# Performance work log

Hardware: AMD Instinct MI355X
Metric: run time of the kernel (lower is better)

Reference implementation:

```python
import jax, jax.numpy as jnp
import numpy as np

N_WIRES = 4
DIM = 2 ** N_WIRES          # 16-dim state vector
N_OPS = 30                  # RandomLayer(n_ops=30)
GAMMA = 1.0
ALPHA = 0.5
C64 = jnp.complex64


def _rx_mat(t):
    h = t / 2
    c = jnp.cos(h).astype(C64)
    s = (-1j * jnp.sin(h)).astype(C64)
    return jnp.stack([jnp.stack([c, s]), jnp.stack([s, c])])


def _ry_mat(t):
    h = t / 2
    c = jnp.cos(h).astype(C64)
    s = jnp.sin(h).astype(C64)
    return jnp.stack([jnp.stack([c, -s]), jnp.stack([s, c])])


def _rz_mat(t):
    h = (t / 2).astype(C64)
    z = jnp.zeros((), C64)
    return jnp.stack([jnp.stack([jnp.exp(-1j * h), z]), jnp.stack([z, jnp.exp(1j * h)])])


def _embed(g, w):
    # kron(I_{2^w}, g, I_{2^{n-1-w}}); wire 0 = most significant qubit
    return jnp.kron(jnp.kron(jnp.eye(2 ** w, dtype=C64), g),
                    jnp.eye(2 ** (N_WIRES - 1 - w), dtype=C64))


def _cnot_full(c, t):
    m = np.zeros((DIM, DIM), np.complex64)
    for i in range(DIM):
        j = i ^ (1 << (N_WIRES - 1 - t)) if (i >> (N_WIRES - 1 - c)) & 1 else i
        m[j, i] = 1.0
    return jnp.asarray(m)


def fixed_unitary(rand_angles, rx_param, ry_param):
    """Compose the whole batch-independent gate sequence (random layer +
    per-wire trainable RX/RY) into one 16x16 unitary — the 'fused kernel'."""
    U = jnp.eye(DIM, dtype=C64)
    for i in range(N_OPS):
        t, w = i % 4, i % N_WIRES
        if t == 0:
            g = _embed(_rx_mat(rand_angles[i]), w)
        elif t == 1:
            g = _embed(_ry_mat(rand_angles[i]), w)
        elif t == 2:
            g = _embed(_rz_mat(rand_angles[i]), w)
        else:
            g = _cnot_full(w, (w + 1) % N_WIRES)
        U = g @ U
    for w in range(N_WIRES):
        U = _embed(_rx_mat(rx_param[0]), w) @ U
        U = _embed(_ry_mat(ry_param[0]), w) @ U
    return U


def encode_ry(state, angles):
    """GeneralEncoder '4xRy': apply RY(angles[:, w]) on wire w, batched."""
    B = state.shape[0]
    for w in range(N_WIRES):
        h = angles[:, w] / 2
        c = jnp.cos(h).astype(C64)[:, None, None]
        s = jnp.sin(h).astype(C64)[:, None, None]
        st = state.reshape(B, 2 ** w, 2, 2 ** (N_WIRES - 1 - w))
        s0, s1 = st[:, :, 0, :], st[:, :, 1, :]
        state = jnp.stack([c * s0 - s * s1, s * s0 + c * s1], axis=2).reshape(B, DIM)
    return state


def setup_inputs() -> dict:
    key = jax.random.key(0)
    k1, k2, k3, k4, k5 = jax.random.split(key, 5)
    B = 1048576
    return {
        "x": jax.random.normal(k1, (B, 4), dtype=jnp.float32),
        "y": jax.random.normal(k2, (B, 4), dtype=jnp.float32),
        "rand_angles": jax.random.uniform(k3, (30,), dtype=jnp.float32),
        "rx_param": jax.random.normal(k4, (1,), dtype=jnp.float32),
        "ry_param": jax.random.normal(k5, (1,), dtype=jnp.float32),
    }


def reference(x, y, rand_angles, rx_param, ry_param):
    B = x.shape[0]
    # classical RBF kernel, [B, 1]
    diff = x - y
    rbf = jnp.exp(-GAMMA * jnp.sum(diff * diff, axis=-1, keepdims=True))
    # quantum kernel: |0..0> -> encode(x) -> fixed unitary -> encode(-y)
    state = jnp.zeros((B, DIM), C64).at[:, 0].set(1.0)
    state = encode_ry(state, x)
    U = fixed_unitary(rand_angles, rx_param, ry_param)
    state = jnp.einsum('ij,bj->bi', U, state)
    state = encode_ry(state, -y)
    # torch: abs(states.view(-1)[0]) — first amplitude of first batch element
    qk = jnp.abs(state.reshape(-1)[0])
    return ALPHA * rbf + (1.0 - ALPHA) * qk
```

## Files before the change

### kernel.cpp

```cpp
#include <hip/hip_runtime.h>
#include <math.h>

#define DIM 16
#define N_OPS 30

__device__ inline float2 cmul(float2 a, float2 b) {
    return make_float2(a.x * b.x - a.y * b.y, a.x * b.y + a.y * b.x);
}
__device__ inline float2 cadd(float2 a, float2 b) {
    return make_float2(a.x + b.x, a.y + b.y);
}

__global__ __launch_bounds__(256) void build_qk_kernel(
    const float* __restrict__ x, const float* __restrict__ y,
    const float* __restrict__ rand_angles, const float* __restrict__ rx_param,
    const float* __restrict__ ry_param, float* __restrict__ qk_out) {
    __shared__ float2 bufA[256];
    __shared__ float2 bufB[256];
    __shared__ float2 stv[DIM];
    __shared__ float2 stv2[DIM];

    const int tid = threadIdx.x;
    const int r = tid >> 4;
    const int c = tid & 15;

    float2* cur = bufA;
    float2* nxt = bufB;

    cur[tid] = make_float2((r == c) ? 1.0f : 0.0f, 0.0f);
    __syncthreads();

    for (int i = 0; i < N_OPS; ++i) {
        const int t = i & 3;
        const int w = i & 3;
        float2 nv;
        if (t < 3) {
            const float h = 0.5f * rand_angles[i];
            const float ch = cosf(h);
            const float sh = sinf(h);
            float2 g00, g01, g10, g11;
            if (t == 0) {
                g00 = make_float2(ch, 0.0f);  g01 = make_float2(0.0f, -sh);
                g10 = make_float2(0.0f, -sh); g11 = make_float2(ch, 0.0f);
            } else if (t == 1) {
                g00 = make_float2(ch, 0.0f);  g01 = make_float2(-sh, 0.0f);
                g10 = make_float2(sh, 0.0f);  g11 = make_float2(ch, 0.0f);
            } else {
                g00 = make_float2(ch, -sh);   g01 = make_float2(0.0f, 0.0f);
                g10 = make_float2(0.0f, 0.0f); g11 = make_float2(ch, sh);
            }
            const int p = 3 - w;
            const int rp = (r >> p) & 1;
            const int r0 = r & ~(1 << p);
            const int r1 = r0 | (1 << p);
            const float2 ga = rp ? g10 : g00;
            const float2 gb = rp ? g11 : g01;
            nv = cadd(cmul(ga, cur[(r0 << 4) | c]), cmul(gb, cur[(r1 << 4) | c]));
        } else {
            const int cw = w;
            const int tw = (w + 1) & 3;
            const int pc = 3 - cw;
            const int pt = 3 - tw;
            const int src = ((r >> pc) & 1) ? (r ^ (1 << pt)) : r;
            nv = cur[(src << 4) | c];
        }
        nxt[tid] = nv;
        __syncthreads();
        float2* tmp = cur; cur = nxt; nxt = tmp;
    }

    const float rxa = rx_param[0];
    const float rya = ry_param[0];
    for (int w = 0; w < 4; ++w) {
        for (int k = 0; k < 2; ++k) {
            const float h = 0.5f * (k == 0 ? rxa : rya);
            const float ch = cosf(h);
            const float sh = sinf(h);
            float2 g00, g01, g10, g11;
            if (k == 0) {
                g00 = make_float2(ch, 0.0f);  g01 = make_float2(0.0f, -sh);
                g10 = make_float2(0.0f, -sh); g11 = make_float2(ch, 0.0f);
            } else {
                g00 = make_float2(ch, 0.0f);  g01 = make_float2(-sh, 0.0f);
                g10 = make_float2(sh, 0.0f);  g11 = make_float2(ch, 0.0f);
            }
            const int p = 3 - w;
            const int rp = (r >> p) & 1;
            const int r0 = r & ~(1 << p);
            const int r1 = r0 | (1 << p);
            const float2 ga = rp ? g10 : g00;
            const float2 gb = rp ? g11 : g01;
            const float2 nv = cadd(cmul(ga, cur[(r0 << 4) | c]), cmul(gb, cur[(r1 << 4) | c]));
            nxt[tid] = nv;
            __syncthreads();
            float2* tmp = cur; cur = nxt; nxt = tmp;
        }
    }

    if (tid == 0) {
        float2 s[DIM];
        for (int i = 0; i < DIM; ++i) s[i] = make_float2(0.0f, 0.0f);
        s[0] = make_float2(1.0f, 0.0f);
        for (int w = 0; w < 4; ++w) {
            const float h = 0.5f * x[w];
            const float ch = cosf(h);
            const float sh = sinf(h);
            const int p = 3 - w;
            for (int r0 = 0; r0 < DIM; ++r0) {
                if ((r0 >> p) & 1) continue;
                const int r1 = r0 | (1 << p);
                const float2 s0 = s[r0];
                const float2 s1 = s[r1];
                s[r0] = make_float2(ch * s0.x - sh * s1.x, ch * s0.y - sh * s1.y);
                s[r1] = make_float2(sh * s0.x + ch * s1.x, sh * s0.y + ch * s1.y);
            }
        }
        for (int i = 0; i < DIM; ++i) stv[i] = s[i];
    }
    __syncthreads();

    if (tid < DIM) {
        float2 acc = make_float2(0.0f, 0.0f);
        for (int cc = 0; cc < DIM; ++cc)
            acc = cadd(acc, cmul(cur[(tid << 4) | cc], stv[cc]));
        stv2[tid] = acc;
    }
    __syncthreads();

    if (tid == 0) {
        float2 s[DIM];
        for (int i = 0; i < DIM; ++i) s[i] = stv2[i];
        for (int w = 0; w < 4; ++w) {
            const float h = -0.5f * y[w];
            const float ch = cosf(h);
            const float sh = sinf(h);
            const int p = 3 - w;
            for (int r0 = 0; r0 < DIM; ++r0) {
                if ((r0 >> p) & 1) continue;
                const int r1 = r0 | (1 << p);
                const float2 s0 = s[r0];
                const float2 s1 = s[r1];
                s[r0] = make_float2(ch * s0.x - sh * s1.x, ch * s0.y - sh * s1.y);
                s[r1] = make_float2(sh * s0.x + ch * s1.x, sh * s0.y + ch * s1.y);
            }
        }
        const float2 a0 = s[0];
        qk_out[0] = sqrtf(a0.x * a0.x + a0.y * a0.y);
    }
}

__global__ __launch_bounds__(256) void rbf_out_kernel(
    const float4* __restrict__ x, const float4* __restrict__ y,
    const float* __restrict__ qk_ptr, float* __restrict__ out, int B) {
    const int idx = blockIdx.x * blockDim.x + threadIdx.x;
    if (idx >= B) return;
    const float half_qk = 0.5f * qk_ptr[0];
    const float4 xv = x[idx];
    const float4 yv = y[idx];
    const float dx = xv.x - yv.x;
    const float dy = xv.y - yv.y;
    const float dz = xv.z - yv.z;
    const float dw = xv.w - yv.w;
    const float ss = dx * dx + dy * dy + dz * dz + dw * dw;
    out[idx] = 0.5f * expf(-ss) + half_qk;
}

extern "C" void kernel_launch(void* const* d_in, const int* in_sizes, int n_in,
                              void* d_out, int out_size, void* d_ws, size_t ws_size,
                              hipStream_t stream) {
    const float* x = (const float*)d_in[0];
    const float* y = (const float*)d_in[1];
    const float* rand_angles = (const float*)d_in[2];
    const float* rx_param = (const float*)d_in[3];
    const float* ry_param = (const float*)d_in[4];
    float* out = (float*)d_out;
    float* qk = (float*)d_ws;

    const int B = in_sizes[0] / 4;

    build_qk_kernel<<<1, 256, 0, stream>>>(x, y, rand_angles, rx_param, ry_param, qk);

    const int blocks = (B + 255) / 256;
    rbf_out_kernel<<<blocks, 256, 0, stream>>>(
        (const float4*)x, (const float4*)y, qk, out, B);
}
```

Measured before the change: 96.26 us.

## Replace 16x16 unitary build with single-wave state-vector simulation via shuffles

Instead of composing the full 16x16 unitary in shared memory with a block barrier after each gate, the setup kernel now simulates only the 16-entry state vector inside one 64-lane wavefront. Gates are applied with cross-lane shuffles, sin/cos are computed once per lane in parallel, and the final overlap with the y-encoding is taken as a shuffle reduction. This removes about 38 __syncthreads and the serial single-thread encode loops from the latency-bound setup kernel. The lane-bit mapping of gates, especially the CNOT handling, is nontrivial and could be wrong, and the large batch RBF kernel is untouched.

```diff
diff --git a/kernel.cpp b/kernel.cpp
--- a/kernel.cpp
+++ b/kernel.cpp
@@ -4,149 +4,98 @@
 #define DIM 16
 #define N_OPS 30
 
-__device__ inline float2 cmul(float2 a, float2 b) {
-    return make_float2(a.x * b.x - a.y * b.y, a.x * b.y + a.y * b.x);
-}
-__device__ inline float2 cadd(float2 a, float2 b) {
-    return make_float2(a.x + b.x, a.y + b.y);
-}
-
-__global__ __launch_bounds__(256) void build_qk_kernel(
+__global__ __launch_bounds__(64) void build_qk_kernel(
     const float* __restrict__ x, const float* __restrict__ y,
     const float* __restrict__ rand_angles, const float* __restrict__ rx_param,
     const float* __restrict__ ry_param, float* __restrict__ qk_out) {
-    __shared__ float2 bufA[256];
-    __shared__ float2 bufB[256];
-    __shared__ float2 stv[DIM];
-    __shared__ float2 stv2[DIM];
+    const int lane = threadIdx.x;
 
-    const int tid = threadIdx.x;
-    const int r = tid >> 4;
-    const int c = tid & 15;
+    float h = 0.0f;
+    if (lane < N_OPS)           h = 0.5f * rand_angles[lane];
+    else if (lane == 30)        h = 0.5f * rx_param[0];
+    else if (lane == 31)        h = 0.5f * ry_param[0];
+    else if (lane >= 32 && lane < 36) h = 0.5f * x[lane - 32];
+    else if (lane >= 36 && lane < 40) h = 0.5f * y[lane - 36];
+    float sh_l, ch_l;
+    __sincosf(h, &sh_l, &ch_l);
 
-    float2* cur = bufA;
-    float2* nxt = bufB;
+    float sr = 1.0f, si = 0.0f;
+    #pragma unroll
+    for (int w = 0; w < 4; ++w) {
+        const int p = 3 - w;
+        const float cw = __shfl(ch_l, 32 + w);
+        const float sw = __shfl(sh_l, 32 + w);
+        sr *= ((lane >> p) & 1) ? sw : cw;
+    }
 
-    cur[tid] = make_float2((r == c) ? 1.0f : 0.0f, 0.0f);
-    __syncthreads();
-
+    #pragma unroll
     for (int i = 0; i < N_OPS; ++i) {
         const int t = i & 3;
-        const int w = i & 3;
-        float2 nv;
-        if (t < 3) {
-            const float h = 0.5f * rand_angles[i];
-            const float ch = cosf(h);
-            const float sh = sinf(h);
-            float2 g00, g01, g10, g11;
-            if (t == 0) {
-                g00 = make_float2(ch, 0.0f);  g01 = make_float2(0.0f, -sh);
-                g10 = make_float2(0.0f, -sh); g11 = make_float2(ch, 0.0f);
-            } else if (t == 1) {
-                g00 = make_float2(ch, 0.0f);  g01 = make_float2(-sh, 0.0f);
-                g10 = make_float2(sh, 0.0f);  g11 = make_float2(ch, 0.0f);
-            } else {
-                g00 = make_float2(ch, -sh);   g01 = make_float2(0.0f, 0.0f);
-                g10 = make_float2(0.0f, 0.0f); g11 = make_float2(ch, sh);
-            }
-            const int p = 3 - w;
-            const int rp = (r >> p) & 1;
-            const int r0 = r & ~(1 << p);
-            const int r1 = r0 | (1 << p);
-            const float2 ga = rp ? g10 : g00;
-            const float2 gb = rp ? g11 : g01;
-            nv = cadd(cmul(ga, cur[(r0 << 4) | c]), cmul(gb, cur[(r1 << 4) | c]));
+        const float ch = __shfl(ch_l, i);
+        const float sh = __shfl(sh_l, i);
+        if (t == 0) {
+            const float pr = __shfl_xor(sr, 8);
+            const float pi = __shfl_xor(si, 8);
+            const float nr = ch * sr + sh * pi;
+            const float ni = ch * si - sh * pr;
+            sr = nr; si = ni;
+        } else if (t == 1) {
+            const float pr = __shfl_xor(sr, 4);
+            const float pi = __shfl_xor(si, 4);
+            const float sg = ((lane >> 2) & 1) ? sh : -sh;
+            const float nr = ch * sr + sg * pr;
+            const float ni = ch * si + sg * pi;
+            sr = nr; si = ni;
+        } else if (t == 2) {
+            const float sg = ((lane >> 1) & 1) ? sh : -sh;
+            const float nr = ch * sr - sg * si;
+            const float ni = ch * si + sg * sr;
+            sr = nr; si = ni;
         } else {
-            const int cw = w;
-            const int tw = (w + 1) & 3;
-            const int pc = 3 - cw;
-            const int pt = 3 - tw;
-            const int src = ((r >> pc) & 1) ? (r ^ (1 << pt)) : r;
-            nv = cur[(src << 4) | c];
-        }
-        nxt[tid] = nv;
-        __syncthreads();
-        float2* tmp = cur; cur = nxt; nxt = tmp;
-    }
-
-    const float rxa = rx_param[0];
-    const float rya = ry_param[0];
-    for (int w = 0; w < 4; ++w) {
-        for (int k = 0; k < 2; ++k) {
-            const float h = 0.5f * (k == 0 ? rxa : rya);
-            const float ch = cosf(h);
-            const float sh = sinf(h);
-            float2 g00, g01, g10, g11;
-            if (k == 0) {
-                g00 = make_float2(ch, 0.0f);  g01 = make_float2(0.0f, -sh);
-                g10 = make_float2(0.0f, -sh); g11 = make_float2(ch, 0.0f);
-            } else {
-                g00 = make_float2(ch, 0.0f);  g01 = make_float2(-sh, 0.0f);
-                g10 = make_float2(sh, 0.0f);  g11 = make_float2(ch, 0.0f);
-            }
-            const int p = 3 - w;
-            const int rp = (r >> p) & 1;
-            const int r0 = r & ~(1 << p);
-            const int r1 = r0 | (1 << p);
-            const float2 ga = rp ? g10 : g00;
-            const float2 gb = rp ? g11 : g01;
-            const float2 nv = cadd(cmul(ga, cur[(r0 << 4) | c]), cmul(gb, cur[(r1 << 4) | c]));
-            nxt[tid] = nv;
-            __syncthreads();
-            float2* tmp = cur; cur = nxt; nxt = tmp;
+            const float pr = __shfl_xor(sr, 8);
+            const float pi = __shfl_xor(si, 8);
+            if (lane & 1) { sr = pr; si = pi; }
         }
     }
 
-    if (tid == 0) {
-        float2 s[DIM];
-        for (int i = 0; i < DIM; ++i) s[i] = make_float2(0.0f, 0.0f);
-        s[0] = make_float2(1.0f, 0.0f);
-        for (int w = 0; w < 4; ++w) {
-            const float h = 0.5f * x[w];
-            const float ch = cosf(h);
-            const float sh = sinf(h);
-            const int p = 3 - w;
-            for (int r0 = 0; r0 < DIM; ++r0) {
-                if ((r0 >> p) & 1) continue;
-                const int r1 = r0 | (1 << p);
-                const float2 s0 = s[r0];
-                const float2 s1 = s[r1];
-                s[r0] = make_float2(ch * s0.x - sh * s1.x, ch * s0.y - sh * s1.y);
-                s[r1] = make_float2(sh * s0.x + ch * s1.x, sh * s0.y + ch * s1.y);
-            }
+    const float chx = __shfl(ch_l, 30), shx = __shfl(sh_l, 30);
+    const float chy = __shfl(ch_l, 31), shy = __shfl(sh_l, 31);
+    #pragma unroll
+    for (int w = 0; w < 4; ++w) {
+        const int p = 3 - w;
+        {
+            const float pr = __shfl_xor(sr, 1 << p);
+            const float pi = __shfl_xor(si, 1 << p);
+            const float nr = chx * sr + shx * pi;
+            const float ni = chx * si - shx * pr;
+            sr = nr; si = ni;
         }
-        for (int i = 0; i < DIM; ++i) stv[i] = s[i];
+        {
+            const float pr = __shfl_xor(sr, 1 << p);
+            const float pi = __shfl_xor(si, 1 << p);
+            const float sg = ((lane >> p) & 1) ? shy : -shy;
+            const float nr = chy * sr + sg * pr;
+            const float ni = chy * si + sg * pi;
+            sr = nr; si = ni;
+        }
     }
-    __syncthreads();
 
-    if (tid < DIM) {
-        float2 acc = make_float2(0.0f, 0.0f);
-        for (int cc = 0; cc < DIM; ++cc)
-            acc = cadd(acc, cmul(cur[(tid << 4) | cc], stv[cc]));
-        stv2[tid] = acc;
+    float wy = 1.0f;
+    #pragma unroll
+    for (int w = 0; w < 4; ++w) {
+        const int p = 3 - w;
+        const float cw = __shfl(ch_l, 36 + w);
+        const float sw = __shfl(sh_l, 36 + w);
+        wy *= ((lane >> p) & 1) ? sw : cw;
     }
-    __syncthreads();
-
-    if (tid == 0) {
-        float2 s[DIM];
-        for (int i = 0; i < DIM; ++i) s[i] = stv2[i];
-        for (int w = 0; w < 4; ++w) {
-            const float h = -0.5f * y[w];
-            const float ch = cosf(h);
-            const float sh = sinf(h);
-            const int p = 3 - w;
-            for (int r0 = 0; r0 < DIM; ++r0) {
-                if ((r0 >> p) & 1) continue;
-                const int r1 = r0 | (1 << p);
-                const float2 s0 = s[r0];
-                const float2 s1 = s[r1];
-                s[r0] = make_float2(ch * s0.x - sh * s1.x, ch * s0.y - sh * s1.y);
-                s[r1] = make_float2(sh * s0.x + ch * s1.x, sh * s0.y + ch * s1.y);
-            }
-        }
-        const float2 a0 = s[0];
-        qk_out[0] = sqrtf(a0.x * a0.x + a0.y * a0.y);
+    float ar = wy * sr;
+    float ai = wy * si;
+    #pragma unroll
+    for (int m = 8; m >= 1; m >>= 1) {
+        ar += __shfl_xor(ar, m);
+        ai += __shfl_xor(ai, m);
     }
+    if (lane == 0) qk_out[0] = sqrtf(ar * ar + ai * ai);
 }
 
 __global__ __launch_bounds__(256) void rbf_out_kernel(
@@ -178,7 +127,7 @@
 
     const int B = in_sizes[0] / 4;
 
-    build_qk_kernel<<<1, 256, 0, stream>>>(x, y, rand_angles, rx_param, ry_param, qk);
+    build_qk_kernel<<<1, 64, 0, stream>>>(x, y, rand_angles, rx_param, ry_param, qk);
 
     const int blocks = (B + 255) / 256;
     rbf_out_kernel<<<blocks, 256, 0, stream>>>(
```

Result: faster. 83.24 us (-13.5%).
